# Kernel tuning notes

Measured on AMD Instinct MI355X. Metric: run time of the kernel, lower is better.

## Reference

```python
import jax, jax.numpy as jnp
import numpy as np

N_NODES = 30000
N_EDGES = 480000
N0, N1 = 64, 16            # hidden irreps: 64x0e (scalars) + 16x1o (vectors)
NUM_LAYERS = 3
NUM_ATOM_TYPES = 100
ATOM_EMB = 64
BOND_DIM, RAD_DIM = 8, 8   # edge_attr_dim=16 -> dim//2 bonded, (dim+1)//2 radial
MAX_RADIUS = 5.0
DEG_NORM = 1.0 / (16.0 ** 0.5)   # 1/sqrt(avg degree), NequIP-style aggregation norm


def soft_one_hot(d, number=RAD_DIM):
    # e3nn soft_one_hot_linspace, basis='gaussian', cutoff=True
    values = jnp.linspace(0.0, MAX_RADIUS, number + 2)[1:-1]
    step = MAX_RADIUS / (number + 1)
    diff = (d[:, None] - values) / step
    return jnp.exp(-diff ** 2) / 1.12


def setup_inputs() -> dict:
    key = jax.random.key(0)
    ks = jax.random.split(key, 16)
    pos = jax.random.normal(ks[0], (N_NODES, 3), jnp.float32) * 2.0
    edge_index = jax.random.randint(ks[1], (2, N_EDGES), 0, N_NODES)
    bond_mask = jax.random.randint(ks[2], (N_EDGES,), 0, 2)
    atom_type = jax.random.randint(ks[3], (N_NODES,), 0, NUM_ATOM_TYPES)

    def p(k, shape, scale):
        return jax.random.normal(k, shape, jnp.float32) * scale

    W_TP = N0 + N1 + N0 + 2 * N1   # per-edge tensor-product path weights (176)
    atom_emb = p(ks[4], (NUM_ATOM_TYPES, ATOM_EMB), 1.0)
    bond_emb = p(ks[5], (2, BOND_DIM), 1.0)
    w_init = p(ks[6], (ATOM_EMB, N0), ATOM_EMB ** -0.5)
    mlp_w1 = p(ks[7], (NUM_LAYERS, BOND_DIM + RAD_DIM, 64), 16 ** -0.5)
    mlp_b1 = jnp.zeros((NUM_LAYERS, 64), jnp.float32)
    mlp_w2 = p(ks[8], (NUM_LAYERS, 64, W_TP), 64 ** -0.5)
    lin_s = p(ks[9], (NUM_LAYERS, N0 + N1, N0), (N0 + N1) ** -0.5)
    lin_v = p(ks[10], (NUM_LAYERS, N0 + 2 * N1, N1), (N0 + 2 * N1) ** -0.5)
    gate_w = p(ks[11], (NUM_LAYERS, N0, N1), N0 ** -0.5)
    hs1 = p(ks[12], (N0, N0), N0 ** -0.5)
    hg = p(ks[13], (N0, N1), N0 ** -0.5)
    hs2 = p(ks[14], (N0, 1), N0 ** -0.5)
    hv2 = p(ks[15], (N1, 1), N1 ** -0.5)
    return dict(pos=pos, edge_index=edge_index, bond_mask=bond_mask,
                atom_type=atom_type, atom_emb=atom_emb, bond_emb=bond_emb,
                w_init=w_init, mlp_w1=mlp_w1, mlp_b1=mlp_b1, mlp_w2=mlp_w2,
                lin_s=lin_s, lin_v=lin_v, gate_w=gate_w,
                hs1=hs1, hg=hg, hs2=hs2, hv2=hv2)


def reference(pos, edge_index, bond_mask, atom_type, atom_emb, bond_emb,
              w_init, mlp_w1, mlp_b1, mlp_w2, lin_s, lin_v, gate_w,
              hs1, hg, hs2, hv2):
    n = pos.shape[0]
    src, dst = edge_index[0], edge_index[1]
    edge_vec = pos[src] - pos[dst]                       # [E,3] irregular gather
    r = jnp.linalg.norm(edge_vec, axis=-1)               # [E]
    u = edge_vec / jnp.maximum(r, 1e-9)[:, None]
    # Spherical harmonics lmax=1, 'component' normalization: Y0=1, Y1=sqrt(3)*r_hat
    y1 = (3.0 ** 0.5) * u                                # [E,3]
    edge_attr = jnp.concatenate([bond_emb[bond_mask], soft_one_hot(r)], axis=-1)  # [E,16]

    s = atom_emb[atom_type] @ w_init                     # [N,N0]; initial_linear (0e only)
    v = jnp.zeros((n, N1, 3), pos.dtype)                 # [N,N1,3]; 1o starts at zero

    for l in range(NUM_LAYERS):
        # radial/edge MLP -> per-edge tensor-product path weights
        w = jax.nn.silu(edge_attr @ mlp_w1[l] + mlp_b1[l]) @ mlp_w2[l]   # [E,176]
        w_ss, w_vs, w_sv, w_vv, w_cx = jnp.split(
            w, [N0, N0 + N1, 2 * N0 + N1, 2 * N0 + 2 * N1], axis=-1)
        se, ve = s[src], v[src]
        # CG tensor-product paths (Y0==1 absorbed):
        #   0e x 0e -> 0e (w_ss), 1o x 1o -> 0e dot (w_vs),
        #   0e x 1o -> 1o (w_sv), 1o x 0e -> 1o (w_vv), 1o x 1o -> 1e~cross (w_cx)
        m_s = jnp.concatenate(
            [w_ss * se, w_vs * jnp.einsum('eic,ec->ei', ve, y1)], axis=-1)  # [E,N0+N1]
        m_v = jnp.concatenate([
            w_sv[:, :, None] * se[:, :, None] * y1[:, None, :],
            w_vv[:, :, None] * ve,
            w_cx[:, :, None] * jnp.cross(ve, y1[:, None, :]),
        ], axis=1)                                       # [E,N0+2*N1,3]
        agg_s = jax.ops.segment_sum(m_s, dst, num_segments=n) * DEG_NORM
        agg_v = jax.ops.segment_sum(m_v, dst, num_segments=n) * DEG_NORM
        out_s = agg_s @ lin_s[l]                         # irrep-wise Linear, 0e
        out_v = jnp.einsum('nic,io->noc', agg_v, lin_v[l])  # irrep-wise Linear, 1o
        # gated nonlinearity + residual self-connection
        s = s + jax.nn.silu(out_s)
        v = v + out_v * jax.nn.sigmoid(out_s @ gate_w[l])[:, :, None]

    # EquivariantMLP output head -> 1x0e + 1x1o per node
    h = jax.nn.silu(s @ hs1)                             # [N,N0]
    vg = v * jax.nn.sigmoid(h @ hg)[:, :, None]          # gated vectors
    pred_s = h @ hs2                                     # [N,1]
    pred_v = jnp.einsum('nic,io->noc', vg, hv2)[:, 0, :] # [N,3]
    return jnp.concatenate([pred_s, pred_v], axis=-1)    # [N,4]
```

## Files before the change

### kernel.cpp

```cpp
#include <hip/hip_runtime.h>
#include <math.h>

#define N_NODES 30000
#define N_EDGES 480000
#define DEGN 0.25f
#define NBLK 1875
#define TPITCH 52

#define FENCE() do { asm volatile("" ::: "memory"); __builtin_amdgcn_sched_barrier(0); } while(0)

typedef __attribute__((ext_vector_type(8))) short short8;
typedef __attribute__((ext_vector_type(4))) float f32x4;

__device__ __forceinline__ float fsilu(float x){ return x / (1.f + __expf(-x)); }
__device__ __forceinline__ float fsig (float x){ return 1.f / (1.f + __expf(-x)); }

__device__ __forceinline__ unsigned bf16rn(float x){
  unsigned u = __float_as_uint(x);
  return (u + 0x7fffu + ((u>>16)&1u)) >> 16;
}
__device__ __forceinline__ unsigned pack2(float a, float b){
  return bf16rn(a) | (bf16rn(b)<<16);
}
__device__ __forceinline__ float bflo(unsigned u){ return __uint_as_float(u<<16); }
__device__ __forceinline__ float bfhi(unsigned u){ return __uint_as_float(u & 0xffff0000u); }

__global__ __launch_bounds__(256) void count2(const int* __restrict__ ei,
                                              int* __restrict__ deg_src,
                                              int* __restrict__ deg_dst)
{
  int e = blockIdx.x*256 + threadIdx.x;
  if (e >= N_EDGES) return;
  atomicAdd(deg_src + ei[e], 1);
  atomicAdd(deg_dst + ei[N_EDGES + e], 1);
}

__global__ __launch_bounds__(1024) void scan_deg2(
    const int* __restrict__ deg_src, int* __restrict__ off_src, int* __restrict__ cur_src,
    const int* __restrict__ deg_dst, int* __restrict__ off_dst, int* __restrict__ cur_dst)
{
  const int* deg = blockIdx.x ? deg_dst : deg_src;
  int* off = blockIdx.x ? off_dst : off_src;
  int* cur = blockIdx.x ? cur_dst : cur_src;
  __shared__ int part[1024];
  int t = threadIdx.x;
  int base = t*30;
  int local[30];
  int s = 0;
  #pragma unroll
  for (int i=0;i<30;i++){
    int idx = base + i;
    int d = (idx < N_NODES) ? deg[idx] : 0;
    local[i] = s; s += d;
  }
  part[t] = s; __syncthreads();
  for (int stp=1; stp<1024; stp<<=1){
    int v = (t >= stp) ? part[t-stp] : 0;
    __syncthreads();
    part[t] += v;
    __syncthreads();
  }
  int prefix = (t==0) ? 0 : part[t-1];
  #pragma unroll
  for (int i=0;i<30;i++){
    int idx = base + i;
    if (idx < N_NODES){ int o = prefix + local[i]; off[idx] = o; cur[idx] = o; }
  }
  if (t == 1023) off[N_NODES] = part[1023];
}

__global__ __launch_bounds__(256) void scatter_src(const int* __restrict__ ei,
                                                   int* __restrict__ cur,
                                                   int* __restrict__ csr_src,
                                                   int* __restrict__ pos_src)
{
  int e = blockIdx.x*256 + threadIdx.x;
  if (e >= N_EDGES) return;
  int p = atomicAdd(cur + ei[e], 1);
  csr_src[p] = e;
  pos_src[e] = p;
}

__global__ __launch_bounds__(256) void scatter_dst(const int* __restrict__ ei,
                                                   const int* __restrict__ pos_src,
                                                   int* __restrict__ cur,
                                                   int* __restrict__ gidx)
{
  int e = blockIdx.x*256 + threadIdx.x;
  if (e >= N_EDGES) return;
  int p = atomicAdd(cur + ei[N_EDGES + e], 1);
  gidx[p] = pos_src[e];
}

__global__ __launch_bounds__(256) void prep_edges2(
    const float* __restrict__ pos, const int* __restrict__ ei,
    const int* __restrict__ bond_mask, const float* __restrict__ bond_emb,
    const int* __restrict__ csr_src, uint4* __restrict__ rec)
{
  int k = blockIdx.x*256 + threadIdx.x;
  if (k >= N_EDGES) return;
  int e = csr_src[k];
  int src = ei[e], dst = ei[N_EDGES + e];
  float ax = pos[src*3+0], ay = pos[src*3+1], az = pos[src*3+2];
  float bx = pos[dst*3+0], by = pos[dst*3+1], bz = pos[dst*3+2];
  float vx = ax-bx, vy = ay-by, vz = az-bz;
  float r = sqrtf(vx*vx + vy*vy + vz*vz);
  float inv = 1.f / fmaxf(r, 1e-9f);
  const float s3 = 1.7320508075688772f;
  float yx = s3*vx*inv, yy = s3*vy*inv, yz = s3*vz*inv;
  int bm = bond_mask[e];
  float eav[16];
  #pragma unroll
  for (int q=0;q<8;q++) eav[q] = bond_emb[bm*8+q];
  const float step = 5.0f/9.0f;
  #pragma unroll
  for (int j=0;j<8;j++){
    float vj = (float)(j+1)*step;
    float d = (r - vj)/step;
    eav[8+j] = __expf(-d*d) * (1.0f/1.12f);
  }
  uint4 r0, r1, r2;
  r0.x = pack2(eav[0],eav[1]);  r0.y = pack2(eav[2],eav[3]);
  r0.z = pack2(eav[4],eav[5]);  r0.w = pack2(eav[6],eav[7]);
  r1.x = pack2(eav[8],eav[9]);  r1.y = pack2(eav[10],eav[11]);
  r1.z = pack2(eav[12],eav[13]);r1.w = pack2(eav[14],eav[15]);
  r2.x = __float_as_uint(yx); r2.y = __float_as_uint(yy);
  r2.z = __float_as_uint(yz); r2.w = (unsigned)src;
  rec[(size_t)k*3+0] = r0;
  rec[(size_t)k*3+1] = r1;
  rec[(size_t)k*3+2] = r2;
}

__global__ void prep_weights(const float* __restrict__ w2,
                             unsigned short* __restrict__ w2hi,
                             unsigned short* __restrict__ w2lo)
{
  int i = blockIdx.x*256 + threadIdx.x;
  if (i >= 3*176*64) return;
  int l = i / (176*64); int rem = i - l*(176*64);
  int n = rem / 64, k = rem - n*64;
  float w = w2[(size_t)l*64*176 + (size_t)k*176 + n];
  unsigned hi = bf16rn(w);
  float lo = w - __uint_as_float(hi<<16);
  w2hi[i] = (unsigned short)hi;
  w2lo[i] = (unsigned short)bf16rn(lo);
}

__global__ __launch_bounds__(256) void init_nodes(
    const int* __restrict__ atom_type, const float* __restrict__ atom_emb,
    const float* __restrict__ w_init, float* __restrict__ s)
{
  int n = blockIdx.x*256 + threadIdx.x;
  if (n >= N_NODES) return;
  int t = atom_type[n];
  float acc[64];
  #pragma unroll
  for (int o=0;o<64;o++) acc[o]=0.f;
  for (int k=0;k<64;k++){
    float ek = atom_emb[t*64+k];
    #pragma unroll
    for (int o=0;o<64;o++) acc[o] = fmaf(ek, w_init[k*64+o], acc[o]);
  }
  float4* so = (float4*)(s + (size_t)n*64);
  #pragma unroll
  for (int q=0;q<16;q++) so[q] = make_float4(acc[4*q],acc[4*q+1],acc[4*q+2],acc[4*q+3]);
}

__device__ __forceinline__ void mfma_tile(
    const unsigned short* __restrict__ W2hi, const unsigned short* __restrict__ W2lo,
    int colbase, const short8 (&bfr)[4][2], int wv, int l, unsigned char* tb)
{
  const unsigned short* ap = W2hi + (size_t)(colbase+(l&15))*64 + ((l>>4)*8);
  const unsigned short* aq = W2lo + (size_t)(colbase+(l&15))*64 + ((l>>4)*8);
  short8 ah0 = *(const short8*)ap;
  short8 ah1 = *(const short8*)(ap+32);
  short8 al0 = *(const short8*)aq;
  short8 al1 = *(const short8*)(aq+32);
  #pragma unroll
  for (int ntg=0;ntg<4;ntg++){
    f32x4 acc = {0.f,0.f,0.f,0.f};
    acc = __builtin_amdgcn_mfma_f32_16x16x32_bf16(ah0, bfr[ntg][0], acc, 0,0,0);
    acc = __builtin_amdgcn_mfma_f32_16x16x32_bf16(ah1, bfr[ntg][1], acc, 0,0,0);
    acc = __builtin_amdgcn_mfma_f32_16x16x32_bf16(al0, bfr[ntg][0], acc, 0,0,0);
    acc = __builtin_amdgcn_mfma_f32_16x16x32_bf16(al1, bfr[ntg][1], acc, 0,0,0);
    int e = wv*64 + ntg*16 + (l&15);
    uint2 pk; pk.x = pack2(acc[0],acc[1]); pk.y = pack2(acc[2],acc[3]);
    *(uint2*)(tb + (size_t)e*TPITCH + ((l>>4)*8)) = pk;
  }
}

__device__ __forceinline__ void decode_w(const unsigned char* tb, int t, float* w)
{
  const unsigned char* wr = tb + (size_t)t*TPITCH;
  uint4 c0 = *(const uint4*)wr;
  uint4 c1 = *(const uint4*)(wr+16);
  w[0]=bflo(c0.x); w[1]=bfhi(c0.x); w[2]=bflo(c0.y); w[3]=bfhi(c0.y);
  w[4]=bflo(c0.z); w[5]=bfhi(c0.z); w[6]=bflo(c0.w); w[7]=bfhi(c0.w);
  w[8]=bflo(c1.x); w[9]=bfhi(c1.x); w[10]=bflo(c1.y); w[11]=bfhi(c1.y);
  w[12]=bflo(c1.z); w[13]=bfhi(c1.z); w[14]=bflo(c1.w); w[15]=bfhi(c1.w);
}

__global__ __launch_bounds__(256)
void edge_fused2(
    const uint4* __restrict__ rec,
    const float* __restrict__ s, const float* __restrict__ v,
    const float* __restrict__ W1,
    const float* __restrict__ b1,
    const unsigned short* __restrict__ W2hi,
    const unsigned short* __restrict__ W2lo,
    const float* __restrict__ linv,
    uint4* __restrict__ msg4)
{
  __shared__ __align__(16) unsigned char lds[59392];
  int t = threadIdx.x;
  int ke = blockIdx.x*256 + t;

  uint4 r0 = rec[(size_t)ke*3+0];
  uint4 r1 = rec[(size_t)ke*3+1];
  uint4 r2 = rec[(size_t)ke*3+2];
  float yx = __uint_as_float(r2.x), yy = __uint_as_float(r2.y), yz = __uint_as_float(r2.z);
  int src = (int)r2.w;

  {
    float eav[16];
    eav[0]=bflo(r0.x); eav[1]=bfhi(r0.x); eav[2]=bflo(r0.y); eav[3]=bfhi(r0.y);
    eav[4]=bflo(r0.z); eav[5]=bfhi(r0.z); eav[6]=bflo(r0.w); eav[7]=bfhi(r0.w);
    eav[8]=bflo(r1.x); eav[9]=bfhi(r1.x); eav[10]=bflo(r1.y); eav[11]=bfhi(r1.y);
    eav[12]=bflo(r1.z); eav[13]=bfhi(r1.z); eav[14]=bflo(r1.w); eav[15]=bfhi(r1.w);
    float h[64];
    #pragma unroll
    for (int k=0;k<64;k++) h[k] = b1[k];
    #pragma unroll
    for (int j=0;j<16;j++){
      float a = eav[j];
      #pragma unroll
      for (int k=0;k<64;k++) h[k] = fmaf(a, W1[j*64+k], h[k]);
    }
    #pragma unroll
    for (int k=0;k<64;k++) h[k] = fsilu(h[k]);
    #pragma unroll
    for (int q=0;q<8;q++){
      uint4 hp;
      hp.x = pack2(h[8*q+0],h[8*q+1]); hp.y = pack2(h[8*q+2],h[8*q+3]);
      hp.z = pack2(h[8*q+4],h[8*q+5]); hp.w = pack2(h[8*q+6],h[8*q+7]);
      int byte = (t*128 + q*16) ^ ((t&7)<<4);
      *(uint4*)(lds + byte) = hp;
    }
  }
  FENCE();

  int wv = t>>6, l = t&63;
  short8 bfr[4][2];
  #pragma unroll
  for (int ntg=0;ntg<4;ntg++){
    int erow = wv*64 + ntg*16 + (l&15);
    #pragma unroll
    for (int kk=0;kk<2;kk++){
      int byte = (erow*128 + kk*64 + ((l>>4)*16)) ^ ((erow&7)<<4);
      bfr[ntg][kk] = *(const short8*)(lds + byte);
    }
  }
  FENCE();

  unsigned char* tbA = lds + 32768;
  unsigned char* tbB = lds + 46080;
  const float* ssrc = s + (size_t)src*64;
  const float4* vsrc4 = (const float4*)(v + (size_t)src*48);
  uint4* mrow = msg4 + ((size_t)(ke>>1))*32 + (ke&1);

  float a_o[16];
  #pragma unroll
  for (int o=0;o<16;o++) a_o[o]=0.f;
  #pragma unroll 1
  for (int st=0; st<4; ++st){
    unsigned char* tb = (st&1) ? tbB : tbA;
    mfma_tile(W2hi, W2lo, 80+st*16, bfr, wv, l, tb);
    FENCE();
    float w[16]; decode_w(tb, t, w);
    int i0 = st*16;
    #pragma unroll
    for (int q4=0;q4<4;q4++){
      float4 s4 = *(const float4*)(ssrc + i0 + q4*4);
      float tq[4] = { w[q4*4+0]*s4.x, w[q4*4+1]*s4.y, w[q4*4+2]*s4.z, w[q4*4+3]*s4.w };
      #pragma unroll
      for (int qq=0;qq<4;qq++){
        int i = i0 + q4*4 + qq;
        float tv = tq[qq];
        #pragma unroll
        for (int o=0;o<16;o++) a_o[o] = fmaf(tv, linv[i*16+o], a_o[o]);
      }
    }
    FENCE();
  }

  mfma_tile(W2hi, W2lo, 144, bfr, wv, l, tbA);
  mfma_tile(W2hi, W2lo, 160, bfr, wv, l, tbB);
  FENCE();
  {
    float wvv[16], wcx[16];
    decode_w(tbA, t, wvv);
    decode_w(tbB, t, wcx);
    #pragma unroll 1
    for (int hf=0; hf<2; ++hf){
      int ob = hf*8;
      float av[24];
      #pragma unroll
      for (int q=0;q<24;q++) av[q]=0.f;
      #pragma unroll
      for (int j4=0;j4<4;j4++){
        float4 a = vsrc4[j4*3+0];
        float4 b = vsrc4[j4*3+1];
        float4 c = vsrc4[j4*3+2];
        float vx_[4] = {a.x, a.w, b.z, c.y};
        float vy_[4] = {a.y, b.x, b.w, c.z};
        float vz_[4] = {a.z, b.y, c.x, c.w};
        #pragma unroll
        for (int jj=0;jj<4;jj++){
          int j = j4*4+jj;
          float cxv = vy_[jj]*yz - vz_[jj]*yy;
          float cyv = vz_[jj]*yx - vx_[jj]*yz;
          float czv = vx_[jj]*yy - vy_[jj]*yx;
          float w1 = wvv[j], w2 = wcx[j];
          #pragma unroll
          for (int o=0;o<8;o++){
            float t1 = w1*linv[(64+j)*16+ob+o];
            float t2 = w2*linv[(80+j)*16+ob+o];
            av[o*3+0] = fmaf(t1, vx_[jj], fmaf(t2, cxv, av[o*3+0]));
            av[o*3+1] = fmaf(t1, vy_[jj], fmaf(t2, cyv, av[o*3+1]));
            av[o*3+2] = fmaf(t1, vz_[jj], fmaf(t2, czv, av[o*3+2]));
          }
        }
      }
      #pragma unroll
      for (int o=0;o<8;o++){
        av[o*3+0] = fmaf(a_o[ob+o], yx, av[o*3+0]);
        av[o*3+1] = fmaf(a_o[ob+o], yy, av[o*3+1]);
        av[o*3+2] = fmaf(a_o[ob+o], yz, av[o*3+2]);
      }
      #pragma unroll
      for (int b2=0;b2<3;b2++){
        uint4 p;
        p.x = pack2(DEGN*av[8*b2+0], DEGN*av[8*b2+1]);
        p.y = pack2(DEGN*av[8*b2+2], DEGN*av[8*b2+3]);
        p.z = pack2(DEGN*av[8*b2+4], DEGN*av[8*b2+5]);
        p.w = pack2(DEGN*av[8*b2+6], DEGN*av[8*b2+7]);
        mrow[(10+hf*3+b2)*2] = p;
      }
    }
  }
  FENCE();

  #pragma unroll 1
  for (int st=0; st<4; ++st){
    unsigned char* tb = (st&1) ? tbB : tbA;
    mfma_tile(W2hi, W2lo, st*16, bfr, wv, l, tb);
    FENCE();
    float w[16]; decode_w(tb, t, w);
    int i0 = st*16;
    float4 s0 = *(const float4*)(ssrc + i0);
    float4 s1 = *(const float4*)(ssrc + i0+4);
    float4 s2 = *(const float4*)(ssrc + i0+8);
    float4 s3 = *(const float4*)(ssrc + i0+12);
    uint4 p0, p1;
    p0.x = pack2(DEGN*w[0]*s0.x, DEGN*w[1]*s0.y);
    p0.y = pack2(DEGN*w[2]*s0.z, DEGN*w[3]*s0.w);
    p0.z = pack2(DEGN*w[4]*s1.x, DEGN*w[5]*s1.y);
    p0.w = pack2(DEGN*w[6]*s1.z, DEGN*w[7]*s1.w);
    p1.x = pack2(DEGN*w[8]*s2.x,  DEGN*w[9]*s2.y);
    p1.y = pack2(DEGN*w[10]*s2.z, DEGN*w[11]*s2.w);
    p1.z = pack2(DEGN*w[12]*s3.x, DEGN*w[13]*s3.y);
    p1.w = pack2(DEGN*w[14]*s3.z, DEGN*w[15]*s3.w);
    mrow[(2*st)*2]   = p0;
    mrow[(2*st+1)*2] = p1;
    FENCE();
  }

  mfma_tile(W2hi, W2lo, 64, bfr, wv, l, tbA);
  FENCE();
  {
    float w[16]; decode_w(tbA, t, w);
    float dv[16];
    #pragma unroll
    for (int j4=0;j4<4;j4++){
      float4 a = vsrc4[j4*3+0];
      float4 b = vsrc4[j4*3+1];
      float4 c = vsrc4[j4*3+2];
      float d0 = a.x*yx + a.y*yy + a.z*yz;
      float d1 = a.w*yx + b.x*yy + b.y*yz;
      float d2 = b.z*yx + b.w*yy + c.x*yz;
      float d3 = c.y*yx + c.z*yy + c.w*yz;
      dv[j4*4+0] = DEGN*w[j4*4+0]*d0;
      dv[j4*4+1] = DEGN*w[j4*4+1]*d1;
      dv[j4*4+2] = DEGN*w[j4*4+2]*d2;
      dv[j4*4+3] = DEGN*w[j4*4+3]*d3;
    }
    uint4 p0, p1;
    p0.x = pack2(dv[0],dv[1]);   p0.y = pack2(dv[2],dv[3]);
    p0.z = pack2(dv[4],dv[5]);   p0.w = pack2(dv[6],dv[7]);
    p1.x = pack2(dv[8],dv[9]);   p1.y = pack2(dv[10],dv[11]);
    p1.z = pack2(dv[12],dv[13]); p1.w = pack2(dv[14],dv[15]);
    mrow[8*2] = p0; mrow[9*2] = p1;
  }
}

__global__ __launch_bounds__(256) void gather_nodes(
    const uint4* __restrict__ msg4,
    const int* __restrict__ off,
    const int* __restrict__ gidx,
    float* __restrict__ agg)
{
  int tid = threadIdx.x;
  int n = blockIdx.x*16 + (tid >> 4);
  int l = tid & 15;
  if (n >= N_NODES) return;
  float acc[8];
  #pragma unroll
  for (int q=0;q<8;q++) acc[q]=0.f;
  int k1 = off[n+1];
  for (int k=off[n]; k<k1; k++){
    int m = gidx[k];
    uint4 mm = msg4[((size_t)(m>>1))*32 + l*2 + (m&1)];
    acc[0] += bflo(mm.x); acc[1] += bfhi(mm.x);
    acc[2] += bflo(mm.y); acc[3] += bfhi(mm.y);
    acc[4] += bflo(mm.z); acc[5] += bfhi(mm.z);
    acc[6] += bflo(mm.w); acc[7] += bfhi(mm.w);
  }
  float4* o = (float4*)(agg + (size_t)n*128 + l*8);
  o[0] = make_float4(acc[0],acc[1],acc[2],acc[3]);
  o[1] = make_float4(acc[4],acc[5],acc[6],acc[7]);
}

__global__ __launch_bounds__(256) void node_update(
    const float* __restrict__ agg,
    const float* __restrict__ lin_s, const float* __restrict__ gate_w,
    float* __restrict__ s, float* __restrict__ v)
{
  int n = blockIdx.x*256 + threadIdx.x;
  if (n >= N_NODES) return;
  const float* row = agg + (size_t)n*128;
  float outs[64];
  #pragma unroll
  for (int o=0;o<64;o++) outs[o]=0.f;
  for (int i=0;i<80;i+=4){
    float4 a4 = *(const float4*)(row + i);
    float av[4]={a4.x,a4.y,a4.z,a4.w};
    #pragma unroll
    for (int q=0;q<4;q++){
      float a = av[q];
      #pragma unroll
      for (int o=0;o<64;o++) outs[o] = fmaf(a, lin_s[(i+q)*64+o], outs[o]);
    }
  }
  float g[16];
  #pragma unroll
  for (int j=0;j<16;j++) g[j]=0.f;
  for (int o=0;o<64;o++){
    float x = outs[o];
    #pragma unroll
    for (int j=0;j<16;j++) g[j] = fmaf(x, gate_w[o*16+j], g[j]);
    s[(size_t)n*64+o] += fsilu(x);
  }
  #pragma unroll
  for (int j=0;j<16;j++){
    float gv = fsig(g[j]);
    v[(size_t)n*48+j*3+0] += row[80+j*3+0]*gv;
    v[(size_t)n*48+j*3+1] += row[80+j*3+1]*gv;
    v[(size_t)n*48+j*3+2] += row[80+j*3+2]*gv;
  }
}

__global__ __launch_bounds__(256) void head_kernel(
    const float* __restrict__ s, const float* __restrict__ v,
    const float* __restrict__ hs1, const float* __restrict__ hg,
    const float* __restrict__ hs2, const float* __restrict__ hv2,
    float* __restrict__ out)
{
  int n = blockIdx.x*256 + threadIdx.x;
  if (n >= N_NODES) return;
  float sv[64];
  const float4* sp = (const float4*)(s + (size_t)n*64);
  #pragma unroll
  for (int q=0;q<16;q++){ float4 t=sp[q]; sv[4*q]=t.x; sv[4*q+1]=t.y; sv[4*q+2]=t.z; sv[4*q+3]=t.w; }
  float h[64];
  #pragma unroll
  for (int o=0;o<64;o++) h[o]=0.f;
  for (int k=0;k<64;k++){
    float x = sv[k];
    #pragma unroll
    for (int o=0;o<64;o++) h[o] = fmaf(x, hs1[k*64+o], h[o]);
  }
  #pragma unroll
  for (int o=0;o<64;o++) h[o] = fsilu(h[o]);
  float g[16];
  #pragma unroll
  for (int j=0;j<16;j++) g[j]=0.f;
  float ps = 0.f;
  for (int o=0;o<64;o++){
    float x = h[o];
    #pragma unroll
    for (int j=0;j<16;j++) g[j] = fmaf(x, hg[o*16+j], g[j]);
    ps = fmaf(x, hs2[o], ps);
  }
  float pvx=0.f, pvy=0.f, pvz=0.f;
  #pragma unroll
  for (int j=0;j<16;j++){
    float gv = fsig(g[j]) * hv2[j];
    pvx = fmaf(v[(size_t)n*48+j*3+0], gv, pvx);
    pvy = fmaf(v[(size_t)n*48+j*3+1], gv, pvy);
    pvz = fmaf(v[(size_t)n*48+j*3+2], gv, pvz);
  }
  *(float4*)(out + (size_t)n*4) = make_float4(ps, pvx, pvy, pvz);
}

extern "C" void kernel_launch(void* const* d_in, const int* in_sizes, int n_in,
                              void* d_out, int out_size, void* d_ws, size_t ws_size,
                              hipStream_t stream)
{
  const float* pos       = (const float*)d_in[0];
  const int*   ei        = (const int*)  d_in[1];
  const int*   bond_mask = (const int*)  d_in[2];
  const int*   atom_type = (const int*)  d_in[3];
  const float* atom_emb  = (const float*)d_in[4];
  const float* bond_emb  = (const float*)d_in[5];
  const float* w_init    = (const float*)d_in[6];
  const float* mlp_w1    = (const float*)d_in[7];
  const float* mlp_b1    = (const float*)d_in[8];
  const float* mlp_w2    = (const float*)d_in[9];
  const float* lin_s     = (const float*)d_in[10];
  const float* lin_v     = (const float*)d_in[11];
  const float* gate_w    = (const float*)d_in[12];
  const float* hs1       = (const float*)d_in[13];
  const float* hg        = (const float*)d_in[14];
  const float* hs2       = (const float*)d_in[15];
  const float* hv2       = (const float*)d_in[16];
  float* out = (float*)d_out;

  char* ws = (char*)d_ws;
  size_t off_b = 0;
  auto alloc = [&](size_t nbytes){ void* p = (void*)(ws + off_b); off_b += ((nbytes + 255)/256)*256; return p; };
  uint4*    rec     = (uint4*)   alloc((size_t)N_EDGES*48);
  uint4*    msg4    = (uint4*)   alloc((size_t)N_EDGES*256);
  float*    sbuf    = (float*)   alloc((size_t)N_NODES*64*4);
  float*    vbuf    = (float*)   alloc((size_t)N_NODES*48*4);
  float*    agg     = (float*)   alloc((size_t)N_NODES*128*4);
  unsigned short* w2hi = (unsigned short*)alloc((size_t)3*176*64*2);
  unsigned short* w2lo = (unsigned short*)alloc((size_t)3*176*64*2);
  int*      deg_src = (int*)     alloc((size_t)N_NODES*4);
  int*      deg_dst = (int*)     alloc((size_t)N_NODES*4);
  int*      off_src = (int*)     alloc((size_t)(N_NODES+1)*4);
  int*      off_dst = (int*)     alloc((size_t)(N_NODES+1)*4);
  int*      cur_src = (int*)     alloc((size_t)N_NODES*4);
  int*      cur_dst = (int*)     alloc((size_t)N_NODES*4);
  int*      csr_src = (int*)     alloc((size_t)N_EDGES*4);
  int*      pos_src = (int*)     alloc((size_t)N_EDGES*4);
  int*      gidx    = (int*)     alloc((size_t)N_EDGES*4);

  dim3 blk(256);
  int gE = (N_EDGES + 255)/256;
  int gN = (N_NODES + 255)/256;
  int gG = (N_NODES + 15)/16;

  hipMemsetAsync(vbuf, 0, (size_t)N_NODES*48*sizeof(float), stream);
  hipMemsetAsync(deg_src, 0, (size_t)2*N_NODES*sizeof(int) + 512, stream);

  count2<<<gE, blk, 0, stream>>>(ei, deg_src, deg_dst);
  scan_deg2<<<2, 1024, 0, stream>>>(deg_src, off_src, cur_src, deg_dst, off_dst, cur_dst);
  scatter_src<<<gE, blk, 0, stream>>>(ei, cur_src, csr_src, pos_src);
  scatter_dst<<<gE, blk, 0, stream>>>(ei, pos_src, cur_dst, gidx);

  prep_edges2<<<gE, blk, 0, stream>>>(pos, ei, bond_mask, bond_emb, csr_src, rec);
  prep_weights<<<(3*176*64 + 255)/256, blk, 0, stream>>>(mlp_w2, w2hi, w2lo);
  init_nodes<<<gN, blk, 0, stream>>>(atom_type, atom_emb, w_init, sbuf);

  for (int l=0;l<3;l++){
    edge_fused2<<<NBLK, blk, 0, stream>>>(rec, sbuf, vbuf,
        mlp_w1 + (size_t)l*16*64, mlp_b1 + (size_t)l*64,
        w2hi + (size_t)l*176*64, w2lo + (size_t)l*176*64,
        lin_v + (size_t)l*96*16,
        msg4);
    gather_nodes<<<gG, blk, 0, stream>>>(msg4, off_dst, gidx, agg);
    node_update<<<gN, blk, 0, stream>>>(agg,
        lin_s + (size_t)l*80*64, gate_w + (size_t)l*64*16, sbuf, vbuf);
  }
  head_kernel<<<gN, blk, 0, stream>>>(sbuf, vbuf, hs1, hg, hs2, hv2, out);
}
```

Before: 1.209 ms.

## Software-pipeline MFMA weight tiles with consumption of previous tile in edge kernel

Splits the MFMA tile routine into A-operand load, MFMA+pack, and LDS store phases, then unrolls the whole sequence of eleven weight tiles. Each stage issues the next tile's global A loads and MFMAs while the VALU consumes the previously decoded tile, ping-ponging between the two LDS buffers. The goal is to hide global load latency and overlap matrix-core work with scalar FMA work. The cost is higher register pressure from the extra live A and accumulator registers, and a longer fully unrolled body.

```diff
diff --git a/kernel.cpp b/kernel.cpp
--- a/kernel.cpp
+++ b/kernel.cpp
@@ -166,26 +166,42 @@
   for (int q=0;q<16;q++) so[q] = make_float4(acc[4*q],acc[4*q+1],acc[4*q+2],acc[4*q+3]);
 }
 
-__device__ __forceinline__ void mfma_tile(
+struct ARegs { short8 h0, h1, l0, l1; };
+
+__device__ __forceinline__ ARegs load_A(
     const unsigned short* __restrict__ W2hi, const unsigned short* __restrict__ W2lo,
-    int colbase, const short8 (&bfr)[4][2], int wv, int l, unsigned char* tb)
-{
+    int colbase, int l)
+{
+  ARegs A;
   const unsigned short* ap = W2hi + (size_t)(colbase+(l&15))*64 + ((l>>4)*8);
   const unsigned short* aq = W2lo + (size_t)(colbase+(l&15))*64 + ((l>>4)*8);
-  short8 ah0 = *(const short8*)ap;
-  short8 ah1 = *(const short8*)(ap+32);
-  short8 al0 = *(const short8*)aq;
-  short8 al1 = *(const short8*)(aq+32);
+  A.h0 = *(const short8*)ap;  A.h1 = *(const short8*)(ap+32);
+  A.l0 = *(const short8*)aq;  A.l1 = *(const short8*)(aq+32);
+  return A;
+}
+
+__device__ __forceinline__ void mfma_pack(const ARegs& A, const short8 (&bfr)[4][2],
+                                          uint2 (&pk)[4])
+{
   #pragma unroll
   for (int ntg=0;ntg<4;ntg++){
     f32x4 acc = {0.f,0.f,0.f,0.f};
-    acc = __builtin_amdgcn_mfma_f32_16x16x32_bf16(ah0, bfr[ntg][0], acc, 0,0,0);
-    acc = __builtin_amdgcn_mfma_f32_16x16x32_bf16(ah1, bfr[ntg][1], acc, 0,0,0);
-    acc = __builtin_amdgcn_mfma_f32_16x16x32_bf16(al0, bfr[ntg][0], acc, 0,0,0);
-    acc = __builtin_amdgcn_mfma_f32_16x16x32_bf16(al1, bfr[ntg][1], acc, 0,0,0);
+    acc = __builtin_amdgcn_mfma_f32_16x16x32_bf16(A.h0, bfr[ntg][0], acc, 0,0,0);
+    acc = __builtin_amdgcn_mfma_f32_16x16x32_bf16(A.h1, bfr[ntg][1], acc, 0,0,0);
+    acc = __builtin_amdgcn_mfma_f32_16x16x32_bf16(A.l0, bfr[ntg][0], acc, 0,0,0);
+    acc = __builtin_amdgcn_mfma_f32_16x16x32_bf16(A.l1, bfr[ntg][1], acc, 0,0,0);
+    pk[ntg].x = pack2(acc[0], acc[1]);
+    pk[ntg].y = pack2(acc[2], acc[3]);
+  }
+}
+
+__device__ __forceinline__ void tile_store(const uint2 (&pk)[4], unsigned char* tb,
+                                           int wv, int l)
+{
+  #pragma unroll
+  for (int ntg=0;ntg<4;ntg++){
     int e = wv*64 + ntg*16 + (l&15);
-    uint2 pk; pk.x = pack2(acc[0],acc[1]); pk.y = pack2(acc[2],acc[3]);
-    *(uint2*)(tb + (size_t)e*TPITCH + ((l>>4)*8)) = pk;
+    *(uint2*)(tb + (size_t)e*TPITCH + ((l>>4)*8)) = pk[ntg];
   }
 }
 
@@ -198,6 +214,43 @@
   w[4]=bflo(c0.z); w[5]=bfhi(c0.z); w[6]=bflo(c0.w); w[7]=bfhi(c0.w);
   w[8]=bflo(c1.x); w[9]=bfhi(c1.x); w[10]=bflo(c1.y); w[11]=bfhi(c1.y);
   w[12]=bflo(c1.z); w[13]=bfhi(c1.z); w[14]=bflo(c1.w); w[15]=bfhi(c1.w);
+}
+
+__device__ __forceinline__ void consume_sv(const float* w, int i0,
+    const float* __restrict__ ssrc, const float* __restrict__ linv, float* a_o)
+{
+  #pragma unroll
+  for (int q4=0;q4<4;q4++){
+    float4 s4 = *(const float4*)(ssrc + i0 + q4*4);
+    float tq[4] = { w[q4*4+0]*s4.x, w[q4*4+1]*s4.y, w[q4*4+2]*s4.z, w[q4*4+3]*s4.w };
+    #pragma unroll
+    for (int qq=0;qq<4;qq++){
+      int i = i0 + q4*4 + qq;
+      float tv = tq[qq];
+      #pragma unroll
+      for (int o=0;o<16;o++) a_o[o] = fmaf(tv, linv[i*16+o], a_o[o]);
+    }
+  }
+}
+
+__device__ __forceinline__ void consume_wss(const float* w, int i0,
+    const float* __restrict__ ssrc, uint4* mrow)
+{
+  float4 s0 = *(const float4*)(ssrc + i0);
+  float4 s1 = *(const float4*)(ssrc + i0+4);
+  float4 s2 = *(const float4*)(ssrc + i0+8);
+  float4 s3 = *(const float4*)(ssrc + i0+12);
+  uint4 p0, p1;
+  p0.x = pack2(DEGN*w[0]*s0.x, DEGN*w[1]*s0.y);
+  p0.y = pack2(DEGN*w[2]*s0.z, DEGN*w[3]*s0.w);
+  p0.z = pack2(DEGN*w[4]*s1.x, DEGN*w[5]*s1.y);
+  p0.w = pack2(DEGN*w[6]*s1.z, DEGN*w[7]*s1.w);
+  p1.x = pack2(DEGN*w[8]*s2.x,  DEGN*w[9]*s2.y);
+  p1.y = pack2(DEGN*w[10]*s2.z, DEGN*w[11]*s2.w);
+  p1.z = pack2(DEGN*w[12]*s3.x, DEGN*w[13]*s3.y);
+  p1.w = pack2(DEGN*w[14]*s3.z, DEGN*w[15]*s3.w);
+  mrow[(i0>>3)*2]     = p0;
+  mrow[((i0>>3)+1)*2] = p1;
 }
 
 __global__ __launch_bounds__(256)
@@ -271,35 +324,38 @@
   float a_o[16];
   #pragma unroll
   for (int o=0;o<16;o++) a_o[o]=0.f;
-  #pragma unroll 1
-  for (int st=0; st<4; ++st){
-    unsigned char* tb = (st&1) ? tbB : tbA;
-    mfma_tile(W2hi, W2lo, 80+st*16, bfr, wv, l, tb);
-    FENCE();
-    float w[16]; decode_w(tb, t, w);
-    int i0 = st*16;
-    #pragma unroll
-    for (int q4=0;q4<4;q4++){
-      float4 s4 = *(const float4*)(ssrc + i0 + q4*4);
-      float tq[4] = { w[q4*4+0]*s4.x, w[q4*4+1]*s4.y, w[q4*4+2]*s4.z, w[q4*4+3]*s4.w };
-      #pragma unroll
-      for (int qq=0;qq<4;qq++){
-        int i = i0 + q4*4 + qq;
-        float tv = tq[qq];
-        #pragma unroll
-        for (int o=0;o<16;o++) a_o[o] = fmaf(tv, linv[i*16+o], a_o[o]);
-      }
-    }
-    FENCE();
-  }
-
-  mfma_tile(W2hi, W2lo, 144, bfr, wv, l, tbA);
-  mfma_tile(W2hi, W2lo, 160, bfr, wv, l, tbB);
-  FENCE();
-  {
-    float wvv[16], wcx[16];
-    decode_w(tbA, t, wvv);
-    decode_w(tbB, t, wcx);
+  uint2 pk[4];
+  float w[16];
+
+  { ARegs A = load_A(W2hi, W2lo, 80, l); mfma_pack(A, bfr, pk); tile_store(pk, tbA, wv, l); }
+  FENCE();
+  { decode_w(tbA, t, w);
+    ARegs A = load_A(W2hi, W2lo, 96, l);
+    consume_sv(w, 0, ssrc, linv, a_o);
+    mfma_pack(A, bfr, pk); tile_store(pk, tbB, wv, l); }
+  FENCE();
+  { decode_w(tbB, t, w);
+    ARegs A = load_A(W2hi, W2lo, 112, l);
+    consume_sv(w, 16, ssrc, linv, a_o);
+    mfma_pack(A, bfr, pk); tile_store(pk, tbA, wv, l); }
+  FENCE();
+  { decode_w(tbA, t, w);
+    ARegs A = load_A(W2hi, W2lo, 128, l);
+    consume_sv(w, 32, ssrc, linv, a_o);
+    mfma_pack(A, bfr, pk); tile_store(pk, tbB, wv, l); }
+  FENCE();
+  { decode_w(tbB, t, w);
+    ARegs A = load_A(W2hi, W2lo, 144, l);
+    consume_sv(w, 48, ssrc, linv, a_o);
+    mfma_pack(A, bfr, pk); tile_store(pk, tbA, wv, l); }
+  FENCE();
+  float wvv[16];
+  { decode_w(tbA, t, wvv);
+    ARegs A = load_A(W2hi, W2lo, 160, l);
+    mfma_pack(A, bfr, pk); tile_store(pk, tbB, wv, l); }
+  FENCE();
+  { decode_w(tbB, t, w);
+    ARegs A = load_A(W2hi, W2lo, 0, l);
     #pragma unroll 1
     for (int hf=0; hf<2; ++hf){
       int ob = hf*8;
@@ -320,7 +376,7 @@
           float cxv = vy_[jj]*yz - vz_[jj]*yy;
           float cyv = vz_[jj]*yx - vx_[jj]*yz;
           float czv = vx_[jj]*yy - vy_[jj]*yx;
-          float w1 = wvv[j], w2 = wcx[j];
+          float w1 = wvv[j], w2 = w[j];
           #pragma unroll
           for (int o=0;o<8;o++){
             float t1 = w1*linv[(64+j)*16+ob+o];
@@ -347,38 +403,29 @@
         mrow[(10+hf*3+b2)*2] = p;
       }
     }
-  }
-  FENCE();
-
-  #pragma unroll 1
-  for (int st=0; st<4; ++st){
-    unsigned char* tb = (st&1) ? tbB : tbA;
-    mfma_tile(W2hi, W2lo, st*16, bfr, wv, l, tb);
-    FENCE();
-    float w[16]; decode_w(tb, t, w);
-    int i0 = st*16;
-    float4 s0 = *(const float4*)(ssrc + i0);
-    float4 s1 = *(const float4*)(ssrc + i0+4);
-    float4 s2 = *(const float4*)(ssrc + i0+8);
-    float4 s3 = *(const float4*)(ssrc + i0+12);
-    uint4 p0, p1;
-    p0.x = pack2(DEGN*w[0]*s0.x, DEGN*w[1]*s0.y);
-    p0.y = pack2(DEGN*w[2]*s0.z, DEGN*w[3]*s0.w);
-    p0.z = pack2(DEGN*w[4]*s1.x, DEGN*w[5]*s1.y);
-    p0.w = pack2(DEGN*w[6]*s1.z, DEGN*w[7]*s1.w);
-    p1.x = pack2(DEGN*w[8]*s2.x,  DEGN*w[9]*s2.y);
-    p1.y = pack2(DEGN*w[10]*s2.z, DEGN*w[11]*s2.w);
-    p1.z = pack2(DEGN*w[12]*s3.x, DEGN*w[13]*s3.y);
-    p1.w = pack2(DEGN*w[14]*s3.z, DEGN*w[15]*s3.w);
-    mrow[(2*st)*2]   = p0;
-    mrow[(2*st+1)*2] = p1;
-    FENCE();
-  }
-
-  mfma_tile(W2hi, W2lo, 64, bfr, wv, l, tbA);
-  FENCE();
-  {
-    float w[16]; decode_w(tbA, t, w);
+    mfma_pack(A, bfr, pk); tile_store(pk, tbA, wv, l); }
+  FENCE();
+  { decode_w(tbA, t, w);
+    ARegs A = load_A(W2hi, W2lo, 16, l);
+    consume_wss(w, 0, ssrc, mrow);
+    mfma_pack(A, bfr, pk); tile_store(pk, tbB, wv, l); }
+  FENCE();
+  { decode_w(tbB, t, w);
+    ARegs A = load_A(W2hi, W2lo, 32, l);
+    consume_wss(w, 16, ssrc, mrow);
+    mfma_pack(A, bfr, pk); tile_store(pk, tbA, wv, l); }
+  FENCE();
+  { decode_w(tbA, t, w);
+    ARegs A = load_A(W2hi, W2lo, 48, l);
+    consume_wss(w, 32, ssrc, mrow);
+    mfma_pack(A, bfr, pk); tile_store(pk, tbB, wv, l); }
+  FENCE();
+  { decode_w(tbB, t, w);
+    ARegs A = load_A(W2hi, W2lo, 64, l);
+    consume_wss(w, 48, ssrc, mrow);
+    mfma_pack(A, bfr, pk); tile_store(pk, tbA, wv, l); }
+  FENCE();
+  { decode_w(tbA, t, w);
     float dv[16];
     #pragma unroll
     for (int j4=0;j4<4;j4++){
```

Result: slower. 3.940 ms (+225.9%).

## Consume MFMA accumulators directly instead of staging weights through LDS

Applied to the files above, without the earlier changes.

The per-edge path-weight MFMA results are now used straight from accumulator registers in the MFMA output layout. Each lane gathers the matching source-node scalar or vector features and shuffles the edge geometry. It writes packed bf16 message fragments directly to global memory, where before the tile went through an LDS staging buffer and was decoded per thread. This removes LDS round trips and barrier-like fences, but it replaces contiguous per-thread row writes with scattered 8-byte stores and extra gathers of node features.

```diff
diff --git a/kernel.cpp b/kernel.cpp
--- a/kernel.cpp
+++ b/kernel.cpp
@@ -352,54 +352,67 @@
 
   #pragma unroll 1
   for (int st=0; st<4; ++st){
-    unsigned char* tb = (st&1) ? tbB : tbA;
-    mfma_tile(W2hi, W2lo, st*16, bfr, wv, l, tb);
+    const unsigned short* ap = W2hi + (size_t)(st*16+(l&15))*64 + ((l>>4)*8);
+    const unsigned short* aq = W2lo + (size_t)(st*16+(l&15))*64 + ((l>>4)*8);
+    short8 ah0 = *(const short8*)ap;
+    short8 ah1 = *(const short8*)(ap+32);
+    short8 al0 = *(const short8*)aq;
+    short8 al1 = *(const short8*)(aq+32);
+    int cb = st*16 + ((l>>4)<<2);
+    #pragma unroll
+    for (int ntg=0;ntg<4;ntg++){
+      f32x4 acc = {0.f,0.f,0.f,0.f};
+      acc = __builtin_amdgcn_mfma_f32_16x16x32_bf16(ah0, bfr[ntg][0], acc, 0,0,0);
+      acc = __builtin_amdgcn_mfma_f32_16x16x32_bf16(ah1, bfr[ntg][1], acc, 0,0,0);
+      acc = __builtin_amdgcn_mfma_f32_16x16x32_bf16(al0, bfr[ntg][0], acc, 0,0,0);
+      acc = __builtin_amdgcn_mfma_f32_16x16x32_bf16(al1, bfr[ntg][1], acc, 0,0,0);
+      int j2 = ntg*16 + (l&15);
+      int src2 = __shfl(src, j2);
+      float4 s4 = *(const float4*)(s + (size_t)src2*64 + cb);
+      uint2 o2;
+      o2.x = pack2(DEGN*acc[0]*s4.x, DEGN*acc[1]*s4.y);
+      o2.y = pack2(DEGN*acc[2]*s4.z, DEGN*acc[3]*s4.w);
+      int ke2 = blockIdx.x*256 + wv*64 + j2;
+      unsigned* mb = (unsigned*)(msg4 + ((size_t)(ke2>>1))*32 + (cb>>3)*2 + (ke2&1));
+      *(uint2*)(mb + ((cb>>2)&1)*2) = o2;
+    }
     FENCE();
-    float w[16]; decode_w(tb, t, w);
-    int i0 = st*16;
-    float4 s0 = *(const float4*)(ssrc + i0);
-    float4 s1 = *(const float4*)(ssrc + i0+4);
-    float4 s2 = *(const float4*)(ssrc + i0+8);
-    float4 s3 = *(const float4*)(ssrc + i0+12);
-    uint4 p0, p1;
-    p0.x = pack2(DEGN*w[0]*s0.x, DEGN*w[1]*s0.y);
-    p0.y = pack2(DEGN*w[2]*s0.z, DEGN*w[3]*s0.w);
-    p0.z = pack2(DEGN*w[4]*s1.x, DEGN*w[5]*s1.y);
-    p0.w = pack2(DEGN*w[6]*s1.z, DEGN*w[7]*s1.w);
-    p1.x = pack2(DEGN*w[8]*s2.x,  DEGN*w[9]*s2.y);
-    p1.y = pack2(DEGN*w[10]*s2.z, DEGN*w[11]*s2.w);
-    p1.z = pack2(DEGN*w[12]*s3.x, DEGN*w[13]*s3.y);
-    p1.w = pack2(DEGN*w[14]*s3.z, DEGN*w[15]*s3.w);
-    mrow[(2*st)*2]   = p0;
-    mrow[(2*st+1)*2] = p1;
-    FENCE();
-  }
-
-  mfma_tile(W2hi, W2lo, 64, bfr, wv, l, tbA);
-  FENCE();
+  }
+
   {
-    float w[16]; decode_w(tbA, t, w);
-    float dv[16];
-    #pragma unroll
-    for (int j4=0;j4<4;j4++){
-      float4 a = vsrc4[j4*3+0];
-      float4 b = vsrc4[j4*3+1];
-      float4 c = vsrc4[j4*3+2];
-      float d0 = a.x*yx + a.y*yy + a.z*yz;
-      float d1 = a.w*yx + b.x*yy + b.y*yz;
-      float d2 = b.z*yx + b.w*yy + c.x*yz;
-      float d3 = c.y*yx + c.z*yy + c.w*yz;
-      dv[j4*4+0] = DEGN*w[j4*4+0]*d0;
-      dv[j4*4+1] = DEGN*w[j4*4+1]*d1;
-      dv[j4*4+2] = DEGN*w[j4*4+2]*d2;
-      dv[j4*4+3] = DEGN*w[j4*4+3]*d3;
-    }
-    uint4 p0, p1;
-    p0.x = pack2(dv[0],dv[1]);   p0.y = pack2(dv[2],dv[3]);
-    p0.z = pack2(dv[4],dv[5]);   p0.w = pack2(dv[6],dv[7]);
-    p1.x = pack2(dv[8],dv[9]);   p1.y = pack2(dv[10],dv[11]);
-    p1.z = pack2(dv[12],dv[13]); p1.w = pack2(dv[14],dv[15]);
-    mrow[8*2] = p0; mrow[9*2] = p1;
+    const unsigned short* ap = W2hi + (size_t)(64+(l&15))*64 + ((l>>4)*8);
+    const unsigned short* aq = W2lo + (size_t)(64+(l&15))*64 + ((l>>4)*8);
+    short8 ah0 = *(const short8*)ap;
+    short8 ah1 = *(const short8*)(ap+32);
+    short8 al0 = *(const short8*)aq;
+    short8 al1 = *(const short8*)(aq+32);
+    int jb = (l>>4)<<2;
+    #pragma unroll
+    for (int ntg=0;ntg<4;ntg++){
+      f32x4 acc = {0.f,0.f,0.f,0.f};
+      acc = __builtin_amdgcn_mfma_f32_16x16x32_bf16(ah0, bfr[ntg][0], acc, 0,0,0);
+      acc = __builtin_amdgcn_mfma_f32_16x16x32_bf16(ah1, bfr[ntg][1], acc, 0,0,0);
+      acc = __builtin_amdgcn_mfma_f32_16x16x32_bf16(al0, bfr[ntg][0], acc, 0,0,0);
+      acc = __builtin_amdgcn_mfma_f32_16x16x32_bf16(al1, bfr[ntg][1], acc, 0,0,0);
+      int j2 = ntg*16 + (l&15);
+      int src2 = __shfl(src, j2);
+      float eyx = __shfl(yx, j2), eyy = __shfl(yy, j2), eyz = __shfl(yz, j2);
+      const float* vp = v + (size_t)src2*48 + jb*3;
+      float4 va = *(const float4*)(vp);
+      float4 vb = *(const float4*)(vp+4);
+      float4 vc = *(const float4*)(vp+8);
+      float d0 = va.x*eyx + va.y*eyy + va.z*eyz;
+      float d1 = va.w*eyx + vb.x*eyy + vb.y*eyz;
+      float d2 = vb.z*eyx + vb.w*eyy + vc.x*eyz;
+      float d3 = vc.y*eyx + vc.z*eyy + vc.w*eyz;
+      uint2 o2;
+      o2.x = pack2(DEGN*acc[0]*d0, DEGN*acc[1]*d1);
+      o2.y = pack2(DEGN*acc[2]*d2, DEGN*acc[3]*d3);
+      int ke2 = blockIdx.x*256 + wv*64 + j2;
+      int i64 = 64 + jb;
+      unsigned* mb = (unsigned*)(msg4 + ((size_t)(ke2>>1))*32 + (i64>>3)*2 + (ke2&1));
+      *(uint2*)(mb + ((i64>>2)&1)*2) = o2;
+    }
   }
 }
 
```

New measurement: 1.173 ms. -2.9%, faster.
